# Kernel tuning notes

Hardware: AMD Instinct MI355X
Metric: run time of the kernel (lower is better)

Reference implementation:

```python
import jax, jax.numpy as jnp
import numpy as np

B, T, H, NEX, ED = 65536, 20, 10, 13, 3

def _p(k, shape):
    return (jax.random.normal(k, shape, jnp.float32) * 0.1)

def setup_inputs() -> dict:
    key = jax.random.key(0)
    ks = jax.random.split(key, 24)
    e = jax.random.randint(ks[0], (B, T), 0, NEX, dtype=jnp.int32)
    f = jax.random.normal(ks[1], (B, T, 3), jnp.float32)
    emb = _p(ks[2], (NEX, ED)).at[0].set(0.0)  # row 0 zeroed as in torch init
    feat_w = _p(ks[3], (3, 3))
    feat_b = _p(ks[4], (3,))
    d = {"e": e, "f": f, "emb": emb, "feat_w": feat_w, "feat_b": feat_b}
    i = 5
    for layer, insz in ((0, 6), (1, 2 * H)):
        for sfx in ("", "r"):
            d[f"w_ih_l{layer}{sfx}"] = _p(ks[i], (4 * H, insz)); i += 1
            d[f"w_hh_l{layer}{sfx}"] = _p(ks[i], (4 * H, H)); i += 1
            d[f"b_ih_l{layer}{sfx}"] = _p(ks[i], (4 * H,)); i += 1
            d[f"b_hh_l{layer}{sfx}"] = _p(ks[i], (4 * H,)); i += 1
    return d

def _lstm_dir(x, w_ih, w_hh, b_ih, b_hh, reverse):
    # x: (B, T, I) -> hidden sequence (B, T, H). PyTorch gate order: i, f, g, o.
    xs = jnp.swapaxes(x, 0, 1)                      # (T, B, I)
    pre = xs @ w_ih.T + (b_ih + b_hh)               # input contribution, (T, B, 4H)
    def step(carry, p):
        h, c = carry
        g = p + h @ w_hh.T
        i, fg, gg, o = jnp.split(g, 4, axis=-1)
        c = jax.nn.sigmoid(fg) * c + jax.nn.sigmoid(i) * jnp.tanh(gg)
        h = jax.nn.sigmoid(o) * jnp.tanh(c)
        return (h, c), h
    nb = x.shape[0]
    init = (jnp.zeros((nb, H), x.dtype), jnp.zeros((nb, H), x.dtype))
    _, hs = jax.lax.scan(step, init, pre, reverse=reverse)
    return jnp.swapaxes(hs, 0, 1)                   # (B, T, H)

def _bilstm_layer(x, pf, pb):
    hf = _lstm_dir(x, *pf, reverse=False)
    hb = _lstm_dir(x, *pb, reverse=True)
    return jnp.concatenate([hf, hb], axis=-1)       # (B, T, 2H)

def reference(e, f, emb, feat_w, feat_b,
              w_ih_l0, w_hh_l0, b_ih_l0, b_hh_l0,
              w_ih_l0r, w_hh_l0r, b_ih_l0r, b_hh_l0r,
              w_ih_l1, w_hh_l1, b_ih_l1, b_hh_l1,
              w_ih_l1r, w_hh_l1r, b_ih_l1r, b_hh_l1r):
    ev = emb[e]                                     # (B, T, 3)
    f3 = f.reshape(-1, T, 3)
    mask = (f3[:, :, 1] != 0).astype(f.dtype)       # (B, T)
    fv = f3 @ feat_w.T + feat_b                     # (B, T, 3)
    x = jnp.concatenate([ev, fv], axis=2)           # (B, T, 6)
    x = _bilstm_layer(x, (w_ih_l0, w_hh_l0, b_ih_l0, b_hh_l0),
                         (w_ih_l0r, w_hh_l0r, b_ih_l0r, b_hh_l0r))
    x = _bilstm_layer(x, (w_ih_l1, w_hh_l1, b_ih_l1, b_hh_l1),
                         (w_ih_l1r, w_hh_l1r, b_ih_l1r, b_hh_l1r))
    ipe = jax.nn.relu(x[:, :, -1] * mask)           # last channel = backward dir unit H-1
    total = ipe.sum(axis=1, keepdims=True)          # (B, 1)
    return (total, ipe)
```

## Files before the change

kernel.cpp:

```cpp
#include <hip/hip_runtime.h>

#define BB 65536
#define TT 20
#define NE 2048
#define FRAG_T 160

#define WS_WGT 0
#define WS_HF0 4096
#define WS_HB0 (WS_HF0 + NE * TT * FRAG_T)
#define WS_END (WS_HB0 + NE * TT * FRAG_T)
#define PK1 0x00003C00u

#define LOG2E  1.442695041f
#define LOG2E2 2.885390082f

typedef unsigned u32;
typedef __fp16 f16x8 __attribute__((ext_vector_type(8)));
typedef float   f32x16 __attribute__((ext_vector_type(16)));
typedef u32     u32x4 __attribute__((ext_vector_type(4)));
typedef __fp16  h2v   __attribute__((ext_vector_type(2)));

__device__ __forceinline__ u32 pk_h16(float a, float b) {
    h2v v = __builtin_amdgcn_cvt_pkrtz(a, b);
    return __builtin_bit_cast(u32, v);
}
__device__ __forceinline__ f32x16 MFMA(u32x4 a, u32x4 b, f32x16 c) {
    return __builtin_amdgcn_mfma_f32_32x32x16_f16(
        __builtin_bit_cast(f16x8, a), __builtin_bit_cast(f16x8, b), c, 0, 0, 0);
}

__device__ __forceinline__ void unit_cr(float ai, float af, float ag, float ao,
                                        float* c, float* h) {
    float pi = __builtin_amdgcn_exp2f(-LOG2E * ai);
    float pf = __builtin_amdgcn_exp2f(-LOG2E * af);
    float q  = __builtin_amdgcn_exp2f(LOG2E2 * ag);
    float fv = __builtin_amdgcn_rcpf(1.0f + pf);
    float ig = (q - 1.0f) * __builtin_amdgcn_rcpf((1.0f + pi) * (q + 1.0f));
    float cv = fmaf(fv, *c, ig);
    *c = cv;
    float po = __builtin_amdgcn_exp2f(-LOG2E * ao);
    float qc = __builtin_amdgcn_exp2f(LOG2E2 * cv);
    *h = (qc - 1.0f) * __builtin_amdgcn_rcpf((1.0f + po) * (qc + 1.0f));
}

__device__ __forceinline__ u32x4 pack_h(const float* h, bool hi, int xaddr, u32 b3) {
    u32 send = hi ? pk_h16(h[3], h[4]) : __float_as_uint(h[4]);
    u32 recv = (u32)__builtin_amdgcn_ds_bpermute(xaddr, (int)send);
    u32 lo0 = pk_h16(h[0], h[1]), lo1 = pk_h16(h[2], h[3]);
    u32 hi0 = pk_h16(__uint_as_float(recv), h[0]);
    u32 hi1 = pk_h16(h[1], h[2]);
    u32x4 b;
    b[0] = hi ? hi0 : lo0;
    b[1] = hi ? hi1 : lo1;
    b[2] = hi ? 0u : recv;
    b[3] = b3;
    return b;
}

__device__ __forceinline__ void cell_update5(const f32x16 a0, const f32x16 a1,
                                             float* c, float* h) {
#pragma unroll
    for (int v = 0; v < 4; ++v)
        unit_cr(a0[v], a0[4 + v], a0[8 + v], a0[12 + v], &c[v], &h[v]);
    unit_cr(a1[0], a1[1], a1[2], a1[3], &c[4], &h[4]);
}

__device__ __forceinline__ int inv_pi(int row) {
    if (row < 32) { int q = row >> 3, rem = row & 7; return q * 10 + 5 * (rem >> 2) + (rem & 3); }
    if (row < 40) { int lo = row - 32; return (lo & 3) * 10 + 5 * (lo >> 2) + 4; }
    return -1;
}

__global__ __launch_bounds__(256)
void prep_mfma(
    const float* __restrict__ wih0, const float* __restrict__ whh0,
    const float* __restrict__ bih0, const float* __restrict__ bhh0,
    const float* __restrict__ wih0r,const float* __restrict__ whh0r,
    const float* __restrict__ bih0r,const float* __restrict__ bhh0r,
    const float* __restrict__ wih1r,const float* __restrict__ whh1r,
    const float* __restrict__ bih1r,const float* __restrict__ bhh1r,
    u32* __restrict__ ws)
{
    for (int gid = threadIdx.x; gid < 14 * 64 * 4; gid += 256) {
        int fid = gid >> 8, l = (gid >> 2) & 63, j = gid & 3;
        int g = l >> 5;
        int tile, chunk;
        if (fid < 8) { tile = (fid >> 1) & 1; chunk = fid & 1; }
        else         { int q = fid - 8; tile = q / 3; chunk = q % 3; }
        int row = tile * 32 + (l & 31);
        int orow = inv_pi(row);
        int kb = (j >> 1) * 8 + 4 * g + (j & 1) * 2;
        float v[2] = {0.f, 0.f};
        if (orow >= 0) {
#pragma unroll
            for (int s = 0; s < 2; ++s) {
                int k = kb + s;
                float val = 0.f;
                if (fid < 8) {
                    bool bwd = fid >= 4;
                    if (chunk == 0) {
                        if (k < 6)       val = (bwd ? wih0r : wih0)[orow * 6 + k];
                        else if (k == 6) val = (bwd ? bih0r[orow] + bhh0r[orow]
                                                    : bih0[orow] + bhh0[orow]);
                    } else {
                        if (k < 10)      val = (bwd ? whh0r : whh0)[orow * 10 + k];
                    }
                } else {
                    if (chunk == 0)      { if (k < 10) val = wih1r[orow * 20 + k]; }
                    else if (chunk == 1) { if (k < 10) val = wih1r[orow * 20 + 10 + k]; }
                    else {
                        if (k < 10)      val = whh1r[orow * 10 + k];
                        else if (k == 10) val = bih1r[orow] + bhh1r[orow];
                    }
                }
                v[s] = val;
            }
        }
        ws[WS_WGT + (fid * 64 + l) * 4 + j] = pk_h16(v[0], v[1]);
    }
}

__global__ __launch_bounds__(64)
void bilstm_l0(
    const int*   __restrict__ eidx, const float* __restrict__ f,
    const float* __restrict__ emb,  const float* __restrict__ fw,
    const float* __restrict__ fb,
    const u32* __restrict__ wsr, u32* __restrict__ ghf, u32* __restrict__ ghb)
{
    __shared__ u32 xs[TT][3][32];
    const int  lane = threadIdx.x;
    const int  e    = lane & 31;
    const bool hi   = lane >= 32;
    const int  wid  = blockIdx.x;
    const int  dir  = wid >> 11;
    const int  eb   = wid & (NE - 1);
    const int  b0   = eb * 32;
    const int  xaddr = (lane ^ 32) << 2;

    {
        float fw0=fw[0],fw1=fw[1],fw2=fw[2],fw3=fw[3],fw4=fw[4];
        float fw5=fw[5],fw6=fw[6],fw7=fw[7],fw8=fw[8];
        float fb0=fb[0],fb1=fb[1],fb2=fb[2];
#pragma unroll 1
        for (int it = 0; it < 10; ++it) {
            int idx = lane + it * 64;
            int ee = idx / 20, t = idx - ee * 20;
            int gi = (b0 + ee) * TT + t;
            float f0 = f[gi * 3], f1 = f[gi * 3 + 1], f2v = f[gi * 3 + 2];
            int ei = eidx[gi] * 3;
            float x0 = emb[ei], x1 = emb[ei + 1], x2 = emb[ei + 2];
            float x3 = fmaf(fw0, f0, fmaf(fw1, f1, fmaf(fw2, f2v, fb0)));
            float x4 = fmaf(fw3, f0, fmaf(fw4, f1, fmaf(fw5, f2v, fb1)));
            float x5 = fmaf(fw6, f0, fmaf(fw7, f1, fmaf(fw8, f2v, fb2)));
            xs[t][0][ee] = pk_h16(x0, x1);
            xs[t][1][ee] = pk_h16(x2, x3);
            xs[t][2][ee] = pk_h16(x4, x5);
        }
    }

    const u32x4* wv = (const u32x4*)wsr;
    const f32x16 zf = {};
    u32* outp = (dir ? ghb : ghf) + (size_t)eb * TT * FRAG_T;
    const int wbase = dir ? 4 : 0;
    u32x4 w0 = wv[(wbase + 0) * 64 + lane], w1 = wv[(wbase + 1) * 64 + lane];
    u32x4 w2 = wv[(wbase + 2) * 64 + lane], w3 = wv[(wbase + 3) * 64 + lane];

    auto BX = [&](int t) {
        u32 x01 = xs[t][0][e], x23 = xs[t][1][e], x45 = xs[t][2][e];
        u32x4 b; b[0] = hi ? x45 : x01; b[1] = hi ? PK1 : x23; b[2] = 0u; b[3] = 0u;
        return b;
    };

    float cst[5] = {0,0,0,0,0}, hv[5] = {0,0,0,0,0};
    const int t0 = dir ? TT - 1 : 0;
    const int dt = dir ? -1 : 1;
    f32x16 a0x = MFMA(w0, BX(t0), zf);
    f32x16 a1x = MFMA(w2, BX(t0), zf);
    u32x4 bh;
#pragma unroll 1
    for (int s = 0; s < TT; ++s) {
        const int t = t0 + s * dt;
        f32x16 a0 = a0x, a1 = a1x;
        if (s > 0) { a0 = MFMA(w1, bh, a0); a1 = MFMA(w3, bh, a1); }
        if (s + 1 < TT) {
            u32x4 bx = BX(t + dt);
            a0x = MFMA(w0, bx, zf);
            a1x = MFMA(w2, bx, zf);
        }
        cell_update5(a0, a1, cst, hv);
        bh = pack_h(hv, hi, xaddr, 0u);
        *(uint2*)(outp + t * FRAG_T + lane * 2) = make_uint2(bh[0], bh[1]);
        if (!hi) outp[t * FRAG_T + 128 + e] = bh[2];
    }
}

__global__ __launch_bounds__(64)
void bilstm_cb(
    const float* __restrict__ f, const u32* __restrict__ wsr,
    const u32* __restrict__ ghf, const u32* __restrict__ ghb,
    float* __restrict__ out)
{
    const int  lane = threadIdx.x;
    const int  e    = lane & 31;
    const bool hi   = lane >= 32;
    const int  eb   = blockIdx.x;
    const int  b0   = eb * 32;
    const int  xaddr = (lane ^ 32) << 2;
    const u32x4* wv = (const u32x4*)wsr;
    u32x4 wB0 = wv[8 * 64 + lane],  wB1 = wv[9 * 64 + lane],  wB2 = wv[10 * 64 + lane];
    u32x4 wB3 = wv[11 * 64 + lane], wB4 = wv[12 * 64 + lane], wB5 = wv[13 * 64 + lane];
    const u32* hfp = ghf + (size_t)eb * TT * FRAG_T;
    const u32* hbp = ghb + (size_t)eb * TT * FRAG_T;
    const f32x16 zf = {};
    float cc[5] = {0,0,0,0,0}, h1v[5] = {0,0,0,0,0}, tot = 0.f;

    uint2 hf2 = *(const uint2*)(hfp + (TT - 1) * FRAG_T + lane * 2);
    u32   hfw = hfp[(TT - 1) * FRAG_T + 128 + e];
    uint2 hb2 = *(const uint2*)(hbp + (TT - 1) * FRAG_T + lane * 2);
    u32   hbw = hbp[(TT - 1) * FRAG_T + 128 + e];
    float f1v = f[((b0 + e) * TT + (TT - 1)) * 3 + 1];

#pragma unroll 1
    for (int t = TT - 1; t >= 0; --t) {
        u32x4 bhf; bhf[0] = hf2.x; bhf[1] = hf2.y; bhf[2] = hi ? 0u : hfw; bhf[3] = 0u;
        u32x4 bhb; bhb[0] = hb2.x; bhb[1] = hb2.y; bhb[2] = hi ? 0u : hbw; bhb[3] = 0u;
        f32x16 B0 = MFMA(wB0, bhf, zf); B0 = MFMA(wB1, bhb, B0);
        f32x16 B1 = MFMA(wB3, bhf, zf); B1 = MFMA(wB4, bhb, B1);
        float fcur = f1v;
        if (t > 0) {
            hf2 = *(const uint2*)(hfp + (t - 1) * FRAG_T + lane * 2);
            hfw = hfp[(t - 1) * FRAG_T + 128 + e];
            hb2 = *(const uint2*)(hbp + (t - 1) * FRAG_T + lane * 2);
            hbw = hbp[(t - 1) * FRAG_T + 128 + e];
            f1v = f[((b0 + e) * TT + (t - 1)) * 3 + 1];
        }
        u32x4 bh1 = pack_h(h1v, hi, xaddr, hi ? 0u : PK1);
        B0 = MFMA(wB2, bh1, B0);
        B1 = MFMA(wB5, bh1, B1);
        cell_update5(B0, B1, cc, h1v);
        if (hi) {
            float ip = fmaxf(h1v[4] * (fcur != 0.f ? 1.f : 0.f), 0.f);
            out[BB + (b0 + e) * TT + t] = ip;
            tot += ip;
        }
    }
    if (hi) out[b0 + e] = tot;
}

template<bool WS> struct Lds {
    u32   x[TT][3][32];
    float m[TT][32];
    u32   hf[WS ? 1 : TT][FRAG_T];
};

template<bool WS>
__global__ __launch_bounds__(64)
void bilstm_mfma(
    const int*   __restrict__ eidx, const float* __restrict__ f,
    const float* __restrict__ emb,  const float* __restrict__ fw,
    const float* __restrict__ fb,
    const u32* __restrict__ wsr, u32* __restrict__ ghf,
    float* __restrict__ out)
{
    __shared__ Lds<WS> lds;
    const int  lane = threadIdx.x;
    const int  e    = lane & 31;
    const bool hi   = lane >= 32;
    const int  wid  = blockIdx.x;
    const int  b0   = wid * 32;
    const int  xaddr = (lane ^ 32) << 2;
    u32* hfp = ghf + (size_t)wid * TT * FRAG_T;

    {
        float fw0=fw[0],fw1=fw[1],fw2=fw[2],fw3=fw[3],fw4=fw[4];
        float fw5=fw[5],fw6=fw[6],fw7=fw[7],fw8=fw[8];
        float fb0=fb[0],fb1=fb[1],fb2=fb[2];
#pragma unroll 1
        for (int it = 0; it < 10; ++it) {
            int idx = lane + it * 64;
            int ee = idx / 20, t = idx - ee * 20;
            int gi = (b0 + ee) * TT + t;
            float f0 = f[gi * 3], f1 = f[gi * 3 + 1], f2v = f[gi * 3 + 2];
            int ei = eidx[gi] * 3;
            float x0 = emb[ei], x1 = emb[ei + 1], x2 = emb[ei + 2];
            float x3 = fmaf(fw0, f0, fmaf(fw1, f1, fmaf(fw2, f2v, fb0)));
            float x4 = fmaf(fw3, f0, fmaf(fw4, f1, fmaf(fw5, f2v, fb1)));
            float x5 = fmaf(fw6, f0, fmaf(fw7, f1, fmaf(fw8, f2v, fb2)));
            lds.x[t][0][ee] = pk_h16(x0, x1);
            lds.x[t][1][ee] = pk_h16(x2, x3);
            lds.x[t][2][ee] = pk_h16(x4, x5);
            lds.m[t][ee]    = (f1 != 0.f) ? 1.f : 0.f;
        }
    }

    const u32x4* wv = (const u32x4*)wsr;
    const f32x16 zf = {};
    {
        u32x4 wf0 = wv[0 * 64 + lane], wf1 = wv[1 * 64 + lane];
        u32x4 wf2 = wv[2 * 64 + lane], wf3 = wv[3 * 64 + lane];
        float cf[5] = {0,0,0,0,0}, hv[5] = {0,0,0,0,0};
        u32x4 bx0;
        {
            u32 x01 = lds.x[0][0][e], x23 = lds.x[0][1][e], x45 = lds.x[0][2][e];
            bx0[0] = hi ? x45 : x01; bx0[1] = hi ? PK1 : x23; bx0[2] = 0u; bx0[3] = 0u;
        }
        f32x16 a0x = MFMA(wf0, bx0, zf);
        f32x16 a1x = MFMA(wf2, bx0, zf);
        u32x4 bh;
#pragma unroll 1
        for (int t = 0; t < TT; ++t) {
            f32x16 a0 = a0x, a1 = a1x;
            if (t > 0) { a0 = MFMA(wf1, bh, a0); a1 = MFMA(wf3, bh, a1); }
            if (t + 1 < TT) {
                u32 x01 = lds.x[t+1][0][e], x23 = lds.x[t+1][1][e], x45 = lds.x[t+1][2][e];
                u32x4 bx; bx[0] = hi ? x45 : x01; bx[1] = hi ? PK1 : x23; bx[2] = 0u; bx[3] = 0u;
                a0x = MFMA(wf0, bx, zf);
                a1x = MFMA(wf2, bx, zf);
            }
            cell_update5(a0, a1, cf, hv);
            bh = pack_h(hv, hi, xaddr, 0u);
            if (WS) {
                *(uint2*)(hfp + t * FRAG_T + lane * 2) = make_uint2(bh[0], bh[1]);
                if (!hi) hfp[t * FRAG_T + 128 + e] = bh[2];
            } else {
                lds.hf[t][lane * 2] = bh[0]; lds.hf[t][lane * 2 + 1] = bh[1];
                if (!hi) lds.hf[t][128 + e] = bh[2];
            }
        }
    }
    {
        u32x4 wb0 = wv[4 * 64 + lane], wb1 = wv[5 * 64 + lane];
        u32x4 wb2 = wv[6 * 64 + lane], wb3 = wv[7 * 64 + lane];
        u32x4 wB0 = wv[8 * 64 + lane], wB1 = wv[9 * 64 + lane], wB2 = wv[10 * 64 + lane];
        u32x4 wB3 = wv[11 * 64 + lane], wB4 = wv[12 * 64 + lane], wB5 = wv[13 * 64 + lane];
        float cb[5] = {0,0,0,0,0}, hbv[5] = {0,0,0,0,0};
        float cc[5] = {0,0,0,0,0}, h1v[5] = {0,0,0,0,0};
        float tot = 0.f;
        {
            u32 x01 = lds.x[TT-1][0][e], x23 = lds.x[TT-1][1][e], x45 = lds.x[TT-1][2][e];
            u32x4 bx; bx[0] = hi ? x45 : x01; bx[1] = hi ? PK1 : x23; bx[2] = 0u; bx[3] = 0u;
            f32x16 a0 = MFMA(wb0, bx, zf);
            f32x16 a1 = MFMA(wb2, bx, zf);
            cell_update5(a0, a1, cb, hbv);
        }
        uint2 cur2; u32 curw;
        if (WS) { cur2 = *(const uint2*)(hfp + (TT-1) * FRAG_T + lane * 2);
                  curw = hfp[(TT-1) * FRAG_T + 128 + e]; }
        else    { cur2 = make_uint2(lds.hf[TT-1][lane * 2], lds.hf[TT-1][lane * 2 + 1]);
                  curw = lds.hf[TT-1][128 + e]; }
#pragma unroll 1
        for (int t = TT - 1; t >= 1; --t) {
            uint2 nxt2; u32 nxtw;
            if (WS) { nxt2 = *(const uint2*)(hfp + (t-1) * FRAG_T + lane * 2);
                      nxtw = hfp[(t-1) * FRAG_T + 128 + e]; }
            else    { nxt2 = make_uint2(lds.hf[t-1][lane * 2], lds.hf[t-1][lane * 2 + 1]);
                      nxtw = lds.hf[t-1][128 + e]; }
            u32x4 shared = pack_h(hbv, hi, xaddr, 0u);
            u32x4 bh1    = pack_h(h1v, hi, xaddr, hi ? 0u : PK1);
            u32x4 bhf; bhf[0] = cur2.x; bhf[1] = cur2.y; bhf[2] = hi ? 0u : curw; bhf[3] = 0u;
            f32x16 B0 = MFMA(wB0, bhf, zf); B0 = MFMA(wB1, shared, B0); B0 = MFMA(wB2, bh1, B0);
            f32x16 B1 = MFMA(wB3, bhf, zf); B1 = MFMA(wB4, shared, B1); B1 = MFMA(wB5, bh1, B1);
            u32 x01 = lds.x[t-1][0][e], x23 = lds.x[t-1][1][e], x45 = lds.x[t-1][2][e];
            u32x4 bx; bx[0] = hi ? x45 : x01; bx[1] = hi ? PK1 : x23; bx[2] = 0u; bx[3] = 0u;
            f32x16 A0 = MFMA(wb0, bx, zf); A0 = MFMA(wb1, shared, A0);
            f32x16 A1 = MFMA(wb2, bx, zf); A1 = MFMA(wb3, shared, A1);
            cell_update5(B0, B1, cc, h1v);
            if (hi) {
                float ip = fmaxf(h1v[4] * lds.m[t][e], 0.f);
                out[BB + (b0 + e) * TT + t] = ip;
                tot += ip;
            }
            cell_update5(A0, A1, cb, hbv);
            cur2 = nxt2; curw = nxtw;
        }
        {
            u32x4 shared = pack_h(hbv, hi, xaddr, 0u);
            u32x4 bh1    = pack_h(h1v, hi, xaddr, hi ? 0u : PK1);
            u32x4 bhf; bhf[0] = cur2.x; bhf[1] = cur2.y; bhf[2] = hi ? 0u : curw; bhf[3] = 0u;
            f32x16 B0 = MFMA(wB0, bhf, zf); B0 = MFMA(wB1, shared, B0); B0 = MFMA(wB2, bh1, B0);
            f32x16 B1 = MFMA(wB3, bhf, zf); B1 = MFMA(wB4, shared, B1); B1 = MFMA(wB5, bh1, B1);
            cell_update5(B0, B1, cc, h1v);
            if (hi) {
                float ip = fmaxf(h1v[4] * lds.m[0][e], 0.f);
                out[BB + (b0 + e) * TT + 0] = ip;
                tot += ip;
                out[b0 + e] = tot;
            }
        }
    }
}

extern "C" void kernel_launch(void* const* d_in, const int* in_sizes, int n_in,
                              void* d_out, int out_size, void* d_ws, size_t ws_size,
                              hipStream_t stream) {
    const int*   eidx  = (const int*)  d_in[0];
    const float* f     = (const float*)d_in[1];
    const float* emb   = (const float*)d_in[2];
    const float* fw    = (const float*)d_in[3];
    const float* fb    = (const float*)d_in[4];
    const float* wih0  = (const float*)d_in[5];
    const float* whh0  = (const float*)d_in[6];
    const float* bih0  = (const float*)d_in[7];
    const float* bhh0  = (const float*)d_in[8];
    const float* wih0r = (const float*)d_in[9];
    const float* whh0r = (const float*)d_in[10];
    const float* bih0r = (const float*)d_in[11];
    const float* bhh0r = (const float*)d_in[12];
    const float* wih1r = (const float*)d_in[17];
    const float* whh1r = (const float*)d_in[18];
    const float* bih1r = (const float*)d_in[19];
    const float* bhh1r = (const float*)d_in[20];
    float* out = (float*)d_out;
    u32* ws = (u32*)d_ws;

    hipLaunchKernelGGL(prep_mfma, dim3(1), dim3(256), 0, stream,
                       wih0, whh0, bih0, bhh0, wih0r, whh0r, bih0r, bhh0r,
                       wih1r, whh1r, bih1r, bhh1r, ws);

    const size_t need_split = (size_t)WS_END * 4;
    const size_t need_r9    = (size_t)(WS_HF0 + (size_t)NE * TT * FRAG_T) * 4;
    if (ws_size >= need_split) {
        hipLaunchKernelGGL(bilstm_l0, dim3(2 * NE), dim3(64), 0, stream,
                           eidx, f, emb, fw, fb, ws, ws + WS_HF0, ws + WS_HB0);
        hipLaunchKernelGGL(bilstm_cb, dim3(NE), dim3(64), 0, stream,
                           f, ws, ws + WS_HF0, ws + WS_HB0, out);
    } else if (ws_size >= need_r9) {
        hipLaunchKernelGGL(bilstm_mfma<true>, dim3(NE), dim3(64), 0, stream,
                           eidx, f, emb, fw, fb, ws, ws + WS_HF0, out);
    } else {
        hipLaunchKernelGGL(bilstm_mfma<false>, dim3(NE), dim3(64), 0, stream,
                           eidx, f, emb, fw, fb, ws, ws + WS_HF0, out);
    }
}
```

Baseline: 78.66 us.

## Fuse layer-0 and layer-1 LSTM kernels into one 4-wave block

Merges the separate layer-0 (fwd/bwd waves) and layer-1 kernels into a single 256-thread block covering two batch groups. Each block builds a shared input tile once, with the mask packed into the B fragment. Waves run the two layer-0 directions in parallel, then after a block barrier one wave per group runs layer 1 from the global scratch. This removes one kernel launch and the redundant reload of f for the mask, at the cost of idling half the waves during layer 1. The middle fallback path is dropped.

```diff
diff --git a/kernel.cpp b/kernel.cpp
--- a/kernel.cpp
+++ b/kernel.cpp
@@ -23,6 +23,9 @@
 __device__ __forceinline__ u32 pk_h16(float a, float b) {
     h2v v = __builtin_amdgcn_cvt_pkrtz(a, b);
     return __builtin_bit_cast(u32, v);
+}
+__device__ __forceinline__ float unpk_hi_f16(u32 u) {
+    return (float)__builtin_bit_cast(h2v, u)[1];
 }
 __device__ __forceinline__ f32x16 MFMA(u32x4 a, u32x4 b, f32x16 c) {
     return __builtin_amdgcn_mfma_f32_32x32x16_f16(
@@ -120,21 +123,25 @@
     }
 }
 
-__global__ __launch_bounds__(64)
-void bilstm_l0(
+struct FusedLds { uint2 bx[2][TT][64]; };
+
+__global__ __launch_bounds__(256, 4)
+void bilstm_fused4(
     const int*   __restrict__ eidx, const float* __restrict__ f,
     const float* __restrict__ emb,  const float* __restrict__ fw,
     const float* __restrict__ fb,
-    const u32* __restrict__ wsr, u32* __restrict__ ghf, u32* __restrict__ ghb)
+    const u32* __restrict__ wsr, u32* __restrict__ ghf, u32* __restrict__ ghb,
+    float* __restrict__ out)
 {
-    __shared__ u32 xs[TT][3][32];
-    const int  lane = threadIdx.x;
+    __shared__ FusedLds lds;
+    const int  tid  = threadIdx.x;
+    const int  lane = tid & 63;
     const int  e    = lane & 31;
     const bool hi   = lane >= 32;
-    const int  wid  = blockIdx.x;
-    const int  dir  = wid >> 11;
-    const int  eb   = wid & (NE - 1);
-    const int  b0   = eb * 32;
+    const int  wslot = __builtin_amdgcn_readfirstlane(tid >> 6);
+    const int  gloc = wslot >> 1;
+    const int  role = wslot & 1;
+    const int  g    = blockIdx.x * 2 + gloc;
     const int  xaddr = (lane ^ 32) << 2;
 
     {
@@ -142,135 +149,120 @@
         float fw5=fw[5],fw6=fw[6],fw7=fw[7],fw8=fw[8];
         float fb0=fb[0],fb1=fb[1],fb2=fb[2];
 #pragma unroll 1
-        for (int it = 0; it < 10; ++it) {
-            int idx = lane + it * 64;
-            int ee = idx / 20, t = idx - ee * 20;
-            int gi = (b0 + ee) * TT + t;
+        for (int it = 0; it < 5; ++it) {
+            int ii = tid + it * 256;
+            int gl = ii / 640, rem = ii - gl * 640;
+            int ee = rem / 20, t = rem - ee * 20;
+            int gi = ((blockIdx.x * 2 + gl) * 32 + ee) * TT + t;
             float f0 = f[gi * 3], f1 = f[gi * 3 + 1], f2v = f[gi * 3 + 2];
             int ei = eidx[gi] * 3;
             float x0 = emb[ei], x1 = emb[ei + 1], x2 = emb[ei + 2];
             float x3 = fmaf(fw0, f0, fmaf(fw1, f1, fmaf(fw2, f2v, fb0)));
             float x4 = fmaf(fw3, f0, fmaf(fw4, f1, fmaf(fw5, f2v, fb1)));
             float x5 = fmaf(fw6, f0, fmaf(fw7, f1, fmaf(fw8, f2v, fb2)));
-            xs[t][0][ee] = pk_h16(x0, x1);
-            xs[t][1][ee] = pk_h16(x2, x3);
-            xs[t][2][ee] = pk_h16(x4, x5);
-        }
-    }
+            float m  = (f1 != 0.f) ? 1.f : 0.f;
+            lds.bx[gl][t][ee]      = make_uint2(pk_h16(x0, x1), pk_h16(x2, x3));
+            lds.bx[gl][t][ee + 32] = make_uint2(pk_h16(x4, x5), pk_h16(1.0f, m));
+        }
+    }
+    __syncthreads();
 
     const u32x4* wv = (const u32x4*)wsr;
     const f32x16 zf = {};
-    u32* outp = (dir ? ghb : ghf) + (size_t)eb * TT * FRAG_T;
-    const int wbase = dir ? 4 : 0;
-    u32x4 w0 = wv[(wbase + 0) * 64 + lane], w1 = wv[(wbase + 1) * 64 + lane];
-    u32x4 w2 = wv[(wbase + 2) * 64 + lane], w3 = wv[(wbase + 3) * 64 + lane];
-
-    auto BX = [&](int t) {
-        u32 x01 = xs[t][0][e], x23 = xs[t][1][e], x45 = xs[t][2][e];
-        u32x4 b; b[0] = hi ? x45 : x01; b[1] = hi ? PK1 : x23; b[2] = 0u; b[3] = 0u;
-        return b;
-    };
-
-    float cst[5] = {0,0,0,0,0}, hv[5] = {0,0,0,0,0};
-    const int t0 = dir ? TT - 1 : 0;
-    const int dt = dir ? -1 : 1;
-    f32x16 a0x = MFMA(w0, BX(t0), zf);
-    f32x16 a1x = MFMA(w2, BX(t0), zf);
-    u32x4 bh;
-#pragma unroll 1
-    for (int s = 0; s < TT; ++s) {
-        const int t = t0 + s * dt;
-        f32x16 a0 = a0x, a1 = a1x;
-        if (s > 0) { a0 = MFMA(w1, bh, a0); a1 = MFMA(w3, bh, a1); }
-        if (s + 1 < TT) {
-            u32x4 bx = BX(t + dt);
-            a0x = MFMA(w0, bx, zf);
-            a1x = MFMA(w2, bx, zf);
-        }
-        cell_update5(a0, a1, cst, hv);
-        bh = pack_h(hv, hi, xaddr, 0u);
-        *(uint2*)(outp + t * FRAG_T + lane * 2) = make_uint2(bh[0], bh[1]);
-        if (!hi) outp[t * FRAG_T + 128 + e] = bh[2];
-    }
-}
-
-__global__ __launch_bounds__(64)
-void bilstm_cb(
-    const float* __restrict__ f, const u32* __restrict__ wsr,
-    const u32* __restrict__ ghf, const u32* __restrict__ ghb,
-    float* __restrict__ out)
-{
-    const int  lane = threadIdx.x;
-    const int  e    = lane & 31;
-    const bool hi   = lane >= 32;
-    const int  eb   = blockIdx.x;
-    const int  b0   = eb * 32;
-    const int  xaddr = (lane ^ 32) << 2;
-    const u32x4* wv = (const u32x4*)wsr;
-    u32x4 wB0 = wv[8 * 64 + lane],  wB1 = wv[9 * 64 + lane],  wB2 = wv[10 * 64 + lane];
-    u32x4 wB3 = wv[11 * 64 + lane], wB4 = wv[12 * 64 + lane], wB5 = wv[13 * 64 + lane];
-    const u32* hfp = ghf + (size_t)eb * TT * FRAG_T;
-    const u32* hbp = ghb + (size_t)eb * TT * FRAG_T;
-    const f32x16 zf = {};
-    float cc[5] = {0,0,0,0,0}, h1v[5] = {0,0,0,0,0}, tot = 0.f;
-
-    uint2 hf2 = *(const uint2*)(hfp + (TT - 1) * FRAG_T + lane * 2);
-    u32   hfw = hfp[(TT - 1) * FRAG_T + 128 + e];
-    uint2 hb2 = *(const uint2*)(hbp + (TT - 1) * FRAG_T + lane * 2);
-    u32   hbw = hbp[(TT - 1) * FRAG_T + 128 + e];
-    float f1v = f[((b0 + e) * TT + (TT - 1)) * 3 + 1];
-
-#pragma unroll 1
-    for (int t = TT - 1; t >= 0; --t) {
-        u32x4 bhf; bhf[0] = hf2.x; bhf[1] = hf2.y; bhf[2] = hi ? 0u : hfw; bhf[3] = 0u;
-        u32x4 bhb; bhb[0] = hb2.x; bhb[1] = hb2.y; bhb[2] = hi ? 0u : hbw; bhb[3] = 0u;
-        f32x16 B0 = MFMA(wB0, bhf, zf); B0 = MFMA(wB1, bhb, B0);
-        f32x16 B1 = MFMA(wB3, bhf, zf); B1 = MFMA(wB4, bhb, B1);
-        float fcur = f1v;
-        if (t > 0) {
-            hf2 = *(const uint2*)(hfp + (t - 1) * FRAG_T + lane * 2);
-            hfw = hfp[(t - 1) * FRAG_T + 128 + e];
-            hb2 = *(const uint2*)(hbp + (t - 1) * FRAG_T + lane * 2);
-            hbw = hbp[(t - 1) * FRAG_T + 128 + e];
-            f1v = f[((b0 + e) * TT + (t - 1)) * 3 + 1];
-        }
-        u32x4 bh1 = pack_h(h1v, hi, xaddr, hi ? 0u : PK1);
-        B0 = MFMA(wB2, bh1, B0);
-        B1 = MFMA(wB5, bh1, B1);
-        cell_update5(B0, B1, cc, h1v);
-        if (hi) {
-            float ip = fmaxf(h1v[4] * (fcur != 0.f ? 1.f : 0.f), 0.f);
-            out[BB + (b0 + e) * TT + t] = ip;
-            tot += ip;
-        }
-    }
-    if (hi) out[b0 + e] = tot;
-}
-
-template<bool WS> struct Lds {
+
+    {
+        const int wbase = role ? 4 : 0;
+        u32x4 w0 = wv[(wbase + 0) * 64 + lane], w1 = wv[(wbase + 1) * 64 + lane];
+        u32x4 w2 = wv[(wbase + 2) * 64 + lane], w3 = wv[(wbase + 3) * 64 + lane];
+        u32* outp = (role ? ghb : ghf) + (size_t)g * TT * FRAG_T;
+        const int t0 = role ? TT - 1 : 0;
+        const int dt = role ? -1 : 1;
+
+        float cst[5] = {0,0,0,0,0}, hv[5] = {0,0,0,0,0};
+        uint2 bw = lds.bx[gloc][t0][lane];
+        u32x4 bx; bx[0] = bw.x; bx[1] = bw.y; bx[2] = 0u; bx[3] = 0u;
+        f32x16 a0x = MFMA(w0, bx, zf);
+        f32x16 a1x = MFMA(w2, bx, zf);
+        u32x4 bh;
+#pragma unroll 1
+        for (int s = 0; s < TT; ++s) {
+            const int t = t0 + s * dt;
+            f32x16 a0 = a0x, a1 = a1x;
+            if (s > 0) { a0 = MFMA(w1, bh, a0); a1 = MFMA(w3, bh, a1); }
+            if (s + 1 < TT) {
+                bw = lds.bx[gloc][t + dt][lane];
+                bx[0] = bw.x; bx[1] = bw.y;
+                a0x = MFMA(w0, bx, zf);
+                a1x = MFMA(w2, bx, zf);
+            }
+            cell_update5(a0, a1, cst, hv);
+            bh = pack_h(hv, hi, xaddr, 0u);
+            *(uint2*)(outp + t * FRAG_T + lane * 2) = make_uint2(bh[0], bh[1]);
+            if (!hi) outp[t * FRAG_T + 128 + e] = bh[2];
+        }
+    }
+    __syncthreads();
+
+    if (role == 0) {
+        u32x4 wB0 = wv[8 * 64 + lane],  wB1 = wv[9 * 64 + lane],  wB2 = wv[10 * 64 + lane];
+        u32x4 wB3 = wv[11 * 64 + lane], wB4 = wv[12 * 64 + lane], wB5 = wv[13 * 64 + lane];
+        const u32* hfp = ghf + (size_t)g * TT * FRAG_T;
+        const u32* hbp = ghb + (size_t)g * TT * FRAG_T;
+        const int b0 = g * 32;
+        float cc[5] = {0,0,0,0,0}, h1v[5] = {0,0,0,0,0}, tot = 0.f;
+
+        uint2 hf2 = *(const uint2*)(hfp + (TT - 1) * FRAG_T + lane * 2);
+        u32   hfw = hfp[(TT - 1) * FRAG_T + 128 + e];
+        uint2 hb2 = *(const uint2*)(hbp + (TT - 1) * FRAG_T + lane * 2);
+        u32   hbw = hbp[(TT - 1) * FRAG_T + 128 + e];
+
+#pragma unroll 1
+        for (int t = TT - 1; t >= 0; --t) {
+            u32x4 bhf; bhf[0] = hf2.x; bhf[1] = hf2.y; bhf[2] = hi ? 0u : hfw; bhf[3] = 0u;
+            u32x4 bhb; bhb[0] = hb2.x; bhb[1] = hb2.y; bhb[2] = hi ? 0u : hbw; bhb[3] = 0u;
+            f32x16 B0 = MFMA(wB0, bhf, zf); B0 = MFMA(wB1, bhb, B0);
+            f32x16 B1 = MFMA(wB3, bhf, zf); B1 = MFMA(wB4, bhb, B1);
+            if (t > 0) {
+                hf2 = *(const uint2*)(hfp + (t - 1) * FRAG_T + lane * 2);
+                hfw = hfp[(t - 1) * FRAG_T + 128 + e];
+                hb2 = *(const uint2*)(hbp + (t - 1) * FRAG_T + lane * 2);
+                hbw = hbp[(t - 1) * FRAG_T + 128 + e];
+            }
+            u32x4 bh1 = pack_h(h1v, hi, xaddr, hi ? 0u : PK1);
+            B0 = MFMA(wB2, bh1, B0);
+            B1 = MFMA(wB5, bh1, B1);
+            cell_update5(B0, B1, cc, h1v);
+            if (hi) {
+                float m  = unpk_hi_f16(lds.bx[gloc][t][lane].y);
+                float ip = fmaxf(h1v[4] * m, 0.f);
+                out[BB + (b0 + e) * TT + t] = ip;
+                tot += ip;
+            }
+        }
+        if (hi) out[b0 + e] = tot;
+    }
+}
+
+struct LdsFB {
     u32   x[TT][3][32];
     float m[TT][32];
-    u32   hf[WS ? 1 : TT][FRAG_T];
+    u32   hf[TT][FRAG_T];
 };
 
-template<bool WS>
 __global__ __launch_bounds__(64)
-void bilstm_mfma(
+void bilstm_fb(
     const int*   __restrict__ eidx, const float* __restrict__ f,
     const float* __restrict__ emb,  const float* __restrict__ fw,
     const float* __restrict__ fb,
-    const u32* __restrict__ wsr, u32* __restrict__ ghf,
-    float* __restrict__ out)
+    const u32* __restrict__ wsr, float* __restrict__ out)
 {
-    __shared__ Lds<WS> lds;
+    __shared__ LdsFB lds;
     const int  lane = threadIdx.x;
     const int  e    = lane & 31;
     const bool hi   = lane >= 32;
     const int  wid  = blockIdx.x;
     const int  b0   = wid * 32;
     const int  xaddr = (lane ^ 32) << 2;
-    u32* hfp = ghf + (size_t)wid * TT * FRAG_T;
-
     {
         float fw0=fw[0],fw1=fw[1],fw2=fw[2],fw3=fw[3],fw4=fw[4];
         float fw5=fw[5],fw6=fw[6],fw7=fw[7],fw8=fw[8];
@@ -292,7 +284,6 @@
             lds.m[t][ee]    = (f1 != 0.f) ? 1.f : 0.f;
         }
     }
-
     const u32x4* wv = (const u32x4*)wsr;
     const f32x16 zf = {};
     {
@@ -319,13 +310,8 @@
             }
             cell_update5(a0, a1, cf, hv);
             bh = pack_h(hv, hi, xaddr, 0u);
-            if (WS) {
-                *(uint2*)(hfp + t * FRAG_T + lane * 2) = make_uint2(bh[0], bh[1]);
-                if (!hi) hfp[t * FRAG_T + 128 + e] = bh[2];
-            } else {
-                lds.hf[t][lane * 2] = bh[0]; lds.hf[t][lane * 2 + 1] = bh[1];
-                if (!hi) lds.hf[t][128 + e] = bh[2];
-            }
+            lds.hf[t][lane * 2] = bh[0]; lds.hf[t][lane * 2 + 1] = bh[1];
+            if (!hi) lds.hf[t][128 + e] = bh[2];
         }
     }
     {
@@ -343,18 +329,12 @@
             f32x16 a1 = MFMA(wb2, bx, zf);
             cell_update5(a0, a1, cb, hbv);
         }
-        uint2 cur2; u32 curw;
-        if (WS) { cur2 = *(const uint2*)(hfp + (TT-1) * FRAG_T + lane * 2);
-                  curw = hfp[(TT-1) * FRAG_T + 128 + e]; }
-        else    { cur2 = make_uint2(lds.hf[TT-1][lane * 2], lds.hf[TT-1][lane * 2 + 1]);
-                  curw = lds.hf[TT-1][128 + e]; }
+        uint2 cur2 = make_uint2(lds.hf[TT-1][lane * 2], lds.hf[TT-1][lane * 2 + 1]);
+        u32   curw = lds.hf[TT-1][128 + e];
 #pragma unroll 1
         for (int t = TT - 1; t >= 1; --t) {
-            uint2 nxt2; u32 nxtw;
-            if (WS) { nxt2 = *(const uint2*)(hfp + (t-1) * FRAG_T + lane * 2);
-                      nxtw = hfp[(t-1) * FRAG_T + 128 + e]; }
-            else    { nxt2 = make_uint2(lds.hf[t-1][lane * 2], lds.hf[t-1][lane * 2 + 1]);
-                      nxtw = lds.hf[t-1][128 + e]; }
+            uint2 nxt2 = make_uint2(lds.hf[t-1][lane * 2], lds.hf[t-1][lane * 2 + 1]);
+            u32   nxtw = lds.hf[t-1][128 + e];
             u32x4 shared = pack_h(hbv, hi, xaddr, 0u);
             u32x4 bh1    = pack_h(h1v, hi, xaddr, hi ? 0u : PK1);
             u32x4 bhf; bhf[0] = cur2.x; bhf[1] = cur2.y; bhf[2] = hi ? 0u : curw; bhf[3] = 0u;
@@ -417,18 +397,11 @@
                        wih0, whh0, bih0, bhh0, wih0r, whh0r, bih0r, bhh0r,
                        wih1r, whh1r, bih1r, bhh1r, ws);
 
-    const size_t need_split = (size_t)WS_END * 4;
-    const size_t need_r9    = (size_t)(WS_HF0 + (size_t)NE * TT * FRAG_T) * 4;
-    if (ws_size >= need_split) {
-        hipLaunchKernelGGL(bilstm_l0, dim3(2 * NE), dim3(64), 0, stream,
-                           eidx, f, emb, fw, fb, ws, ws + WS_HF0, ws + WS_HB0);
-        hipLaunchKernelGGL(bilstm_cb, dim3(NE), dim3(64), 0, stream,
-                           f, ws, ws + WS_HF0, ws + WS_HB0, out);
-    } else if (ws_size >= need_r9) {
-        hipLaunchKernelGGL(bilstm_mfma<true>, dim3(NE), dim3(64), 0, stream,
-                           eidx, f, emb, fw, fb, ws, ws + WS_HF0, out);
+    if (ws_size >= (size_t)WS_END * 4) {
+        hipLaunchKernelGGL(bilstm_fused4, dim3(NE / 2), dim3(256), 0, stream,
+                           eidx, f, emb, fw, fb, ws, ws + WS_HF0, ws + WS_HB0, out);
     } else {
-        hipLaunchKernelGGL(bilstm_mfma<false>, dim3(NE), dim3(64), 0, stream,
-                           eidx, f, emb, fw, fb, ws, ws + WS_HF0, out);
-    }
-}
+        hipLaunchKernelGGL(bilstm_fb, dim3(NE), dim3(64), 0, stream,
+                           eidx, f, emb, fw, fb, ws, out);
+    }
+}
```

Result: faster. 71.97 us (-8.5%).
